# Kernel tuning notes

Measured on AMD Instinct MI355X. Metric: run time of the kernel, lower is better.

## Reference

```python
import jax, jax.numpy as jnp
import numpy as np
import math

NUM_HEADS = 8  # init kwarg num_heads


def setup_inputs() -> dict:
    key = jax.random.key(0)
    k1, k2, k3, k4, k5 = jax.random.split(key, 5)
    n, q, kv, d, W = 2048, 256, 256, 64, 64  # n = batch(4) * windows(64) * heads(8)
    return {
        "queries": jax.random.normal(k1, (n, q, d), jnp.float32),
        "keys": jax.random.normal(k2, (n, kv, d), jnp.float32),
        "values": jax.random.normal(k3, (n, kv, d), jnp.float32),
        "valid_lens": jax.random.randint(k5, (n,), 0, 256, jnp.int32),
        "window_mask": jax.random.normal(k4, (W, q, kv), jnp.float32),
    }


def reference(queries, keys, values, valid_lens, window_mask):
    d = queries.shape[-1]
    # scores = Q K^T / sqrt(d)
    scores = jnp.einsum('bqd,bkd->bqk', queries, keys) / math.sqrt(d)
    n, q, kv = scores.shape
    W = window_mask.shape[0]
    # additive Swin-style window mask, broadcast over batch and heads
    scores = (scores.reshape(n // (W * NUM_HEADS), W, NUM_HEADS, q, kv)
              + window_mask[None, :, None]).reshape(n, q, kv)
    # masked softmax: multiply valid entries, add -1e6 to invalid (matches _sequence_mask)
    mask = (jnp.arange(kv)[None, None, :] < valid_lens[:, None, None]).astype(scores.dtype)
    scores = scores * mask + (1.0 - mask) * (-1e6)
    attn = jax.nn.softmax(scores, axis=-1)
    # dropout p=0.0 -> identity
    return jnp.einsum('bqk,bkd->bqd', attn, values)
```

## Files before the change

kernel.cpp:

```cpp
#include <hip/hip_runtime.h>
#include <stdint.h>

typedef __attribute__((ext_vector_type(8))) short short8;
typedef __attribute__((ext_vector_type(4))) float floatx4;

#define SEQQ 256
#define SEQK 256
#define HD   64
#define KSTR 72
#define VTSTR 264
#define PSTR 40

__device__ __forceinline__ uint32_t rpack2(float a, float b) {
    uint32_t ua = __builtin_bit_cast(uint32_t, a) + 0x8000u;
    uint32_t ub = __builtin_bit_cast(uint32_t, b) + 0x8000u;
    return __builtin_amdgcn_perm(ub, ua, 0x07060302u);
}
__device__ __forceinline__ unsigned short f2b(float x) {
    return (unsigned short)((__builtin_bit_cast(uint32_t, x) + 0x8000u) >> 16);
}
__device__ __forceinline__ float b2f(unsigned short b) {
    return __builtin_bit_cast(float, ((uint32_t)b) << 16);
}

__global__ __launch_bounds__(256) void wm_convert(const float* __restrict__ wm,
                                                  unsigned short* __restrict__ out) {
    int i = (blockIdx.x * 256 + threadIdx.x) * 8;
    float4 a = *(const float4*)(wm + i);
    float4 b = *(const float4*)(wm + i + 4);
    uint4 o;
    o.x = rpack2(a.x, a.y); o.y = rpack2(a.z, a.w);
    o.z = rpack2(b.x, b.y); o.w = rpack2(b.z, b.w);
    *(uint4*)(out + i) = o;
}

template <bool WMBF16>
__global__ __launch_bounds__(256) void attn_fused(
    const float* __restrict__ Qg, const float* __restrict__ Kg,
    const float* __restrict__ Vg, const int* __restrict__ Lg,
    const void* __restrict__ WMg, float* __restrict__ Og)
{
    __shared__ __align__(16) unsigned short ldsKV[SEQK * KSTR];
    __shared__ __align__(16) unsigned short ldsP[4 * 2 * 16 * PSTR];

    const int tid   = threadIdx.x;
    const int lane  = tid & 63;
    const int wave  = tid >> 6;
    const int row16 = lane & 15;
    const int quad  = lane >> 4;

    const int bidx  = blockIdx.x;
    const int batch = bidx >> 2;
    const int qb    = bidx & 3;
    const int q0    = qb * 64 + wave * 16;

    const float* qptr = Qg + (size_t)batch * SEQQ * HD;
    const float* kptr = Kg + (size_t)batch * SEQK * HD;
    const float* vptr = Vg + (size_t)batch * SEQK * HD;
    const size_t wmoff = (size_t)((batch >> 3) & 63) * SEQQ * SEQK;
    const int L = Lg[batch];

    #pragma unroll
    for (int it = 0; it < 16; ++it) {
        int pe  = it * 256 + tid;
        int kvr = pe >> 4;
        int pi  = pe & 15;
        const float4 f = *(const float4*)(kptr + kvr * HD + pi * 4);
        uint2 pk; pk.x = rpack2(f.x, f.y); pk.y = rpack2(f.z, f.w);
        *(uint2*)&ldsKV[kvr * KSTR + pi * 4] = pk;
    }

    short8 qf0, qf1;
    {
        const float* qr = qptr + (q0 + row16) * HD + quad * 8;
        float4 a = *(const float4*)(qr);
        float4 b = *(const float4*)(qr + 4);
        float4 c = *(const float4*)(qr + 32);
        float4 d = *(const float4*)(qr + 36);
        union { short8 s; uint32_t u[4]; } t0, t1;
        t0.u[0] = rpack2(a.x, a.y); t0.u[1] = rpack2(a.z, a.w);
        t0.u[2] = rpack2(b.x, b.y); t0.u[3] = rpack2(b.z, b.w);
        t1.u[0] = rpack2(c.x, c.y); t1.u[1] = rpack2(c.z, c.w);
        t1.u[2] = rpack2(d.x, d.y); t1.u[3] = rpack2(d.z, d.w);
        qf0 = t0.s; qf1 = t1.s;
    }

    __syncthreads();

    floatx4 acc[16];
    #pragma unroll
    for (int j = 0; j < 16; ++j) acc[j] = (floatx4){0.f, 0.f, 0.f, 0.f};
    #pragma unroll
    for (int j = 0; j < 16; ++j) {
        const unsigned short* kb = &ldsKV[(j * 16 + row16) * KSTR + quad * 8];
        short8 kf0 = *(const short8*)kb;
        short8 kf1 = *(const short8*)(kb + 32);
        acc[j] = __builtin_amdgcn_mfma_f32_16x16x32_bf16(qf0, kf0, acc[j], 0, 0, 0);
        acc[j] = __builtin_amdgcn_mfma_f32_16x16x32_bf16(qf1, kf1, acc[j], 0, 0, 0);
    }

    __syncthreads();

    #pragma unroll 4
    for (int it = 0; it < 16; ++it) {
        int p4 = it * 256 + tid;
        int d  = p4 & 63;
        int kv = (p4 >> 6) * 4;
        float v0 = vptr[(kv + 0) * HD + d];
        float v1 = vptr[(kv + 1) * HD + d];
        float v2 = vptr[(kv + 2) * HD + d];
        float v3 = vptr[(kv + 3) * HD + d];
        uint2 pk; pk.x = rpack2(v0, v1); pk.y = rpack2(v2, v3);
        *(uint2*)&ldsKV[d * VTSTR + kv] = pk;
    }

    float inv[4];
    #pragma unroll
    for (int r = 0; r < 4; ++r) {
        const int qrow = q0 + quad * 4 + r;
        float wv[16];
        if (WMBF16) {
            const unsigned short* wr = (const unsigned short*)WMg + wmoff + qrow * SEQK + row16;
            #pragma unroll
            for (int j = 0; j < 16; ++j) wv[j] = b2f(wr[16 * j]);
        } else {
            const float* wr = (const float*)WMg + wmoff + qrow * SEQK + row16;
            #pragma unroll
            for (int j = 0; j < 16; ++j) wv[j] = wr[16 * j];
        }
        float mx = -3.0e38f;
        #pragma unroll
        for (int j = 0; j < 16; ++j) {
            float s = acc[j][r] * 0.125f + wv[j];
            s = (16 * j + row16 < L) ? s : -1.0e6f;
            acc[j][r] = s;
            mx = fmaxf(mx, s);
        }
        #pragma unroll
        for (int o = 1; o < 16; o <<= 1) mx = fmaxf(mx, __shfl_xor(mx, o, 64));
        float sm = 0.f;
        #pragma unroll
        for (int j = 0; j < 16; ++j) {
            float e = exp2f((acc[j][r] - mx) * 1.44269504088896f);
            acc[j][r] = e;
            sm += e;
        }
        #pragma unroll
        for (int o = 1; o < 16; o <<= 1) sm += __shfl_xor(sm, o, 64);
        inv[r] = __builtin_amdgcn_rcpf(sm);
    }

    __syncthreads();

    floatx4 oacc[4];
    #pragma unroll
    for (int t = 0; t < 4; ++t) oacc[t] = (floatx4){0.f, 0.f, 0.f, 0.f};
    unsigned short* psbase = &ldsP[wave * 2 * 16 * PSTR];
    #pragma unroll
    for (int c = 0; c < 8; ++c) {
        unsigned short* ps = psbase + (c & 1) * 16 * PSTR;
        #pragma unroll
        for (int r = 0; r < 4; ++r) {
            const int prow = quad * 4 + r;
            ps[prow * PSTR + row16]      = f2b(acc[2 * c    ][r] * inv[r]);
            ps[prow * PSTR + 16 + row16] = f2b(acc[2 * c + 1][r] * inv[r]);
        }
        __asm__ __volatile__("" ::: "memory");
        __builtin_amdgcn_s_waitcnt(0xC07F);
        short8 pf = *(const short8*)&ps[row16 * PSTR + quad * 8];
        #pragma unroll
        for (int t = 0; t < 4; ++t) {
            short8 vf = *(const short8*)&ldsKV[(t * 16 + row16) * VTSTR + c * 32 + quad * 8];
            oacc[t] = __builtin_amdgcn_mfma_f32_16x16x32_bf16(pf, vf, oacc[t], 0, 0, 0);
        }
    }

    float* op = Og + (size_t)batch * SEQQ * HD;
    #pragma unroll
    for (int t = 0; t < 4; ++t) {
        #pragma unroll
        for (int r = 0; r < 4; ++r) {
            op[(q0 + quad * 4 + r) * HD + t * 16 + row16] = oacc[t][r];
        }
    }
}

extern "C" void kernel_launch(void* const* d_in, const int* in_sizes, int n_in,
                              void* d_out, int out_size, void* d_ws, size_t ws_size,
                              hipStream_t stream) {
    const float* Qg = (const float*)d_in[0];
    const float* Kg = (const float*)d_in[1];
    const float* Vg = (const float*)d_in[2];
    const int*   Lg = (const int*)d_in[3];
    const float* Wm = (const float*)d_in[4];
    float* Og = (float*)d_out;

    const int nbatch = in_sizes[3];
    const int wm_elems = in_sizes[4];
    dim3 block(256);

    if ((size_t)wm_elems * sizeof(unsigned short) <= ws_size) {
        unsigned short* wmb = (unsigned short*)d_ws;
        hipLaunchKernelGGL(wm_convert, dim3(wm_elems / 2048), block, 0, stream, Wm, wmb);
        hipLaunchKernelGGL((attn_fused<true>), dim3(nbatch * 4), block, 0, stream,
                           Qg, Kg, Vg, Lg, (const void*)wmb, Og);
    } else {
        hipLaunchKernelGGL((attn_fused<false>), dim3(nbatch * 4), block, 0, stream,
                           Qg, Kg, Vg, Lg, (const void*)Wm, Og);
    }
}
```

Before: 472.6 us.

## Process 128 query rows per block with 8 waves and defer softmax normalization

After: 681.4 us. 1.44x slower.

```diff
diff --git a/kernel.cpp b/kernel.cpp
--- a/kernel.cpp
+++ b/kernel.cpp
@@ -10,6 +10,7 @@
 #define KSTR 72
 #define VTSTR 264
 #define PSTR 40
+#define NW   8
 
 __device__ __forceinline__ uint32_t rpack2(float a, float b) {
     uint32_t ua = __builtin_bit_cast(uint32_t, a) + 0x8000u;
@@ -25,23 +26,23 @@
 
 __global__ __launch_bounds__(256) void wm_convert(const float* __restrict__ wm,
                                                   unsigned short* __restrict__ out) {
+    const float LG2E = 1.44269504088896f;
     int i = (blockIdx.x * 256 + threadIdx.x) * 8;
     float4 a = *(const float4*)(wm + i);
     float4 b = *(const float4*)(wm + i + 4);
     uint4 o;
-    o.x = rpack2(a.x, a.y); o.y = rpack2(a.z, a.w);
-    o.z = rpack2(b.x, b.y); o.w = rpack2(b.z, b.w);
+    o.x = rpack2(a.x * LG2E, a.y * LG2E); o.y = rpack2(a.z * LG2E, a.w * LG2E);
+    o.z = rpack2(b.x * LG2E, b.y * LG2E); o.w = rpack2(b.z * LG2E, b.w * LG2E);
     *(uint4*)(out + i) = o;
 }
 
-template <bool WMBF16>
-__global__ __launch_bounds__(256) void attn_fused(
+__global__ __launch_bounds__(512, 6) void attn_fused(
     const float* __restrict__ Qg, const float* __restrict__ Kg,
     const float* __restrict__ Vg, const int* __restrict__ Lg,
-    const void* __restrict__ WMg, float* __restrict__ Og)
+    const unsigned short* __restrict__ WMg, float* __restrict__ Og)
 {
     __shared__ __align__(16) unsigned short ldsKV[SEQK * KSTR];
-    __shared__ __align__(16) unsigned short ldsP[4 * 2 * 16 * PSTR];
+    __shared__ __align__(16) unsigned short ldsP[NW * 16 * PSTR];
 
     const int tid   = threadIdx.x;
     const int lane  = tid & 63;
@@ -50,19 +51,19 @@
     const int quad  = lane >> 4;
 
     const int bidx  = blockIdx.x;
-    const int batch = bidx >> 2;
-    const int qb    = bidx & 3;
-    const int q0    = qb * 64 + wave * 16;
+    const int batch = bidx >> 1;
+    const int qh    = bidx & 1;
+    const int q0    = qh * 128 + wave * 16;
 
     const float* qptr = Qg + (size_t)batch * SEQQ * HD;
     const float* kptr = Kg + (size_t)batch * SEQK * HD;
     const float* vptr = Vg + (size_t)batch * SEQK * HD;
-    const size_t wmoff = (size_t)((batch >> 3) & 63) * SEQQ * SEQK;
+    const unsigned short* wptr = WMg + (size_t)((batch >> 3) & 63) * SEQQ * SEQK;
     const int L = Lg[batch];
 
     #pragma unroll
-    for (int it = 0; it < 16; ++it) {
-        int pe  = it * 256 + tid;
+    for (int it = 0; it < 8; ++it) {
+        int pe  = it * 512 + tid;
         int kvr = pe >> 4;
         int pi  = pe & 15;
         const float4 f = *(const float4*)(kptr + kvr * HD + pi * 4);
@@ -101,37 +102,32 @@
 
     __syncthreads();
 
-    #pragma unroll 4
-    for (int it = 0; it < 16; ++it) {
-        int p4 = it * 256 + tid;
-        int d  = p4 & 63;
-        int kv = (p4 >> 6) * 4;
-        float v0 = vptr[(kv + 0) * HD + d];
-        float v1 = vptr[(kv + 1) * HD + d];
-        float v2 = vptr[(kv + 2) * HD + d];
-        float v3 = vptr[(kv + 3) * HD + d];
-        uint2 pk; pk.x = rpack2(v0, v1); pk.y = rpack2(v2, v3);
-        *(uint2*)&ldsKV[d * VTSTR + kv] = pk;
+    #pragma unroll
+    for (int it = 0; it < 4; ++it) {
+        int u  = it * 512 + tid;
+        int d4 = (u & 15) * 4;
+        int kv = (u >> 4) * 2;
+        const float4 a = *(const float4*)(vptr + kv * HD + d4);
+        const float4 b = *(const float4*)(vptr + (kv + 1) * HD + d4);
+        *(uint32_t*)&ldsKV[(d4 + 0) * VTSTR + kv] = rpack2(a.x, b.x);
+        *(uint32_t*)&ldsKV[(d4 + 1) * VTSTR + kv] = rpack2(a.y, b.y);
+        *(uint32_t*)&ldsKV[(d4 + 2) * VTSTR + kv] = rpack2(a.z, b.z);
+        *(uint32_t*)&ldsKV[(d4 + 3) * VTSTR + kv] = rpack2(a.w, b.w);
     }
 
     float inv[4];
+    const float SC = 0.125f * 1.44269504088896f;
     #pragma unroll
     for (int r = 0; r < 4; ++r) {
         const int qrow = q0 + quad * 4 + r;
+        const unsigned short* wr = wptr + qrow * SEQK + row16;
         float wv[16];
-        if (WMBF16) {
-            const unsigned short* wr = (const unsigned short*)WMg + wmoff + qrow * SEQK + row16;
-            #pragma unroll
-            for (int j = 0; j < 16; ++j) wv[j] = b2f(wr[16 * j]);
-        } else {
-            const float* wr = (const float*)WMg + wmoff + qrow * SEQK + row16;
-            #pragma unroll
-            for (int j = 0; j < 16; ++j) wv[j] = wr[16 * j];
-        }
+        #pragma unroll
+        for (int j = 0; j < 16; ++j) wv[j] = b2f(wr[16 * j]);
         float mx = -3.0e38f;
         #pragma unroll
         for (int j = 0; j < 16; ++j) {
-            float s = acc[j][r] * 0.125f + wv[j];
+            float s = acc[j][r] * SC + wv[j];
             s = (16 * j + row16 < L) ? s : -1.0e6f;
             acc[j][r] = s;
             mx = fmaxf(mx, s);
@@ -141,7 +137,7 @@
         float sm = 0.f;
         #pragma unroll
         for (int j = 0; j < 16; ++j) {
-            float e = exp2f((acc[j][r] - mx) * 1.44269504088896f);
+            float e = __builtin_amdgcn_exp2f(acc[j][r] - mx);
             acc[j][r] = e;
             sm += e;
         }
@@ -155,15 +151,14 @@
     floatx4 oacc[4];
     #pragma unroll
     for (int t = 0; t < 4; ++t) oacc[t] = (floatx4){0.f, 0.f, 0.f, 0.f};
-    unsigned short* psbase = &ldsP[wave * 2 * 16 * PSTR];
+    unsigned short* ps = &ldsP[wave * 16 * PSTR];
     #pragma unroll
     for (int c = 0; c < 8; ++c) {
-        unsigned short* ps = psbase + (c & 1) * 16 * PSTR;
         #pragma unroll
         for (int r = 0; r < 4; ++r) {
             const int prow = quad * 4 + r;
-            ps[prow * PSTR + row16]      = f2b(acc[2 * c    ][r] * inv[r]);
-            ps[prow * PSTR + 16 + row16] = f2b(acc[2 * c + 1][r] * inv[r]);
+            ps[prow * PSTR + row16]      = f2b(acc[2 * c    ][r]);
+            ps[prow * PSTR + 16 + row16] = f2b(acc[2 * c + 1][r]);
         }
         __asm__ __volatile__("" ::: "memory");
         __builtin_amdgcn_s_waitcnt(0xC07F);
@@ -173,6 +168,7 @@
             short8 vf = *(const short8*)&ldsKV[(t * 16 + row16) * VTSTR + c * 32 + quad * 8];
             oacc[t] = __builtin_amdgcn_mfma_f32_16x16x32_bf16(pf, vf, oacc[t], 0, 0, 0);
         }
+        __asm__ __volatile__("" ::: "memory");
     }
 
     float* op = Og + (size_t)batch * SEQQ * HD;
@@ -180,7 +176,7 @@
     for (int t = 0; t < 4; ++t) {
         #pragma unroll
         for (int r = 0; r < 4; ++r) {
-            op[(q0 + quad * 4 + r) * HD + t * 16 + row16] = oacc[t][r];
+            op[(q0 + quad * 4 + r) * HD + t * 16 + row16] = oacc[t][r] * inv[r];
         }
     }
 }
@@ -197,15 +193,9 @@
 
     const int nbatch = in_sizes[3];
     const int wm_elems = in_sizes[4];
-    dim3 block(256);
-
-    if ((size_t)wm_elems * sizeof(unsigned short) <= ws_size) {
-        unsigned short* wmb = (unsigned short*)d_ws;
-        hipLaunchKernelGGL(wm_convert, dim3(wm_elems / 2048), block, 0, stream, Wm, wmb);
-        hipLaunchKernelGGL((attn_fused<true>), dim3(nbatch * 4), block, 0, stream,
-                           Qg, Kg, Vg, Lg, (const void*)wmb, Og);
-    } else {
-        hipLaunchKernelGGL((attn_fused<false>), dim3(nbatch * 4), block, 0, stream,
-                           Qg, Kg, Vg, Lg, (const void*)Wm, Og);
-    }
-}
+
+    unsigned short* wmb = (unsigned short*)d_ws;
+    hipLaunchKernelGGL(wm_convert, dim3(wm_elems / 2048), dim3(256), 0, stream, Wm, wmb);
+    hipLaunchKernelGGL(attn_fused, dim3(nbatch * 2), dim3(512), 0, stream,
+                       Qg, Kg, Vg, Lg, wmb, Og);
+}
```
